# Kernel tuning notes

Hardware: AMD Instinct MI355X
Metric: run time of the kernel (lower is better)

The kernel has to match this reference:

```python
import jax, jax.numpy as jnp
import numpy as np

N = 100000       # nodes
E = 1600000      # edges (avg degree 16)
ND = 64          # node_dim
ED = 1           # edge_dim
HD = 128         # hidden_dim of message MLP


def setup_inputs() -> dict:
    key = jax.random.key(0)
    ks = jax.random.split(key, 12)
    x = jax.random.normal(ks[0], (N, ND), dtype=jnp.float32)
    edge_index = jax.random.randint(ks[1], (2, E), 0, N, dtype=jnp.int32)
    edge_attr = jax.random.normal(ks[2], (E, ED), dtype=jnp.float32)
    # message_net: Linear(2*ND+ED -> HD), ReLU, Linear(HD -> ND); torch default uniform init
    s1 = 1.0 / np.sqrt(2 * ND + ED)
    W1 = jax.random.uniform(ks[3], (HD, 2 * ND + ED), minval=-s1, maxval=s1, dtype=jnp.float32)
    b1 = jax.random.uniform(ks[4], (HD,), minval=-s1, maxval=s1, dtype=jnp.float32)
    s2 = 1.0 / np.sqrt(HD)
    W2 = jax.random.uniform(ks[5], (ND, HD), minval=-s2, maxval=s2, dtype=jnp.float32)
    b2 = jax.random.uniform(ks[6], (ND,), minval=-s2, maxval=s2, dtype=jnp.float32)
    # GRUCell(input=ND, hidden=ND): weight_ih [3*ND, ND], weight_hh [3*ND, ND]
    sg = 1.0 / np.sqrt(ND)
    W_ih = jax.random.uniform(ks[7], (3 * ND, ND), minval=-sg, maxval=sg, dtype=jnp.float32)
    b_ih = jax.random.uniform(ks[8], (3 * ND,), minval=-sg, maxval=sg, dtype=jnp.float32)
    W_hh = jax.random.uniform(ks[9], (3 * ND, ND), minval=-sg, maxval=sg, dtype=jnp.float32)
    b_hh = jax.random.uniform(ks[10], (3 * ND,), minval=-sg, maxval=sg, dtype=jnp.float32)
    return {"x": x, "edge_index": edge_index, "edge_attr": edge_attr,
            "W1": W1, "b1": b1, "W2": W2, "b2": b2,
            "W_ih": W_ih, "b_ih": b_ih, "W_hh": W_hh, "b_hh": b_hh}


def reference(x, edge_index, edge_attr, W1, b1, W2, b2, W_ih, b_ih, W_hh, b_hh):
    src, dst = edge_index[0], edge_index[1]
    # gather + concat + 2-layer MLP message  -> [E, ND]
    m = jnp.concatenate([x[src], x[dst], edge_attr], axis=-1)      # [E, 2*ND+ED]
    m = jax.nn.relu(m @ W1.T + b1) @ W2.T + b2                     # [E, ND]
    # scatter-add aggregate to destination nodes
    aggr = jnp.zeros_like(x).at[dst].add(m)                        # [N, ND]
    # torch GRUCell: input=aggr, hidden=x
    gi = aggr @ W_ih.T + b_ih                                      # [N, 3*ND]
    gh = x @ W_hh.T + b_hh                                         # [N, 3*ND]
    i_r, i_z, i_n = jnp.split(gi, 3, axis=-1)
    h_r, h_z, h_n = jnp.split(gh, 3, axis=-1)
    r = jax.nn.sigmoid(i_r + h_r)
    z = jax.nn.sigmoid(i_z + h_z)
    n = jnp.tanh(i_n + r * h_n)
    return (1.0 - z) * n + z * x
```

## Files before the change

kernel.cpp:

```cpp
#include <hip/hip_runtime.h>

#define NN 100000
#define NE 1600000
#define ND 64
#define HD 128
#define NPB 8
#define NBK (NN / NPB)
#define NPCB 400
#define NCB 250
#define NFPC (NPCB / NPB)
#define NBA 64
#define CHA (NE / NBA)
#define MSC (NCB * NBA)
#define CSC 16

typedef float f32x4 __attribute__((ext_vector_type(4)));
typedef short s16x8 __attribute__((ext_vector_type(8)));


static __device__ __forceinline__ short f2bf(float f) {
    union { float f; unsigned u; } v; v.f = f;
    unsigned r = (v.u + 0x7fffu + ((v.u >> 16) & 1u)) >> 16;
    return (short)r;
}

#define LSW(n, k)  (((n) << 7) + ((((k) >> 3) ^ ((n) & 15)) << 3) + ((k) & 7))
#define LSW64(n, k) (((n) << 6) + ((((k) >> 3) ^ ((n) & 7)) << 3) + ((k) & 7))

__global__ __launch_bounds__(1024) void histA(const int* __restrict__ ei,
                                              int* __restrict__ gHistA,
                                              const float* __restrict__ x,
                                              short* __restrict__ xb) {
    __shared__ int h[NCB];
    const int tid = threadIdx.x;
    if (tid < NCB) h[tid] = 0;
    __syncthreads();
    const int base = blockIdx.x * CHA;
    for (int i = tid; i < CHA; i += 1024)
        atomicAdd(&h[ei[NE + base + i] / NPCB], 1);
    __syncthreads();
    if (tid < NCB) gHistA[tid * NBA + blockIdx.x] = h[tid];

    const int NG = NN * ND / 8;
    for (int g = blockIdx.x * 1024 + tid; g < NG; g += NBA * 1024) {
        const float4 a = ((const float4*)x)[g * 2];
        const float4 b = ((const float4*)x)[g * 2 + 1];
        s16x8 o;
        o[0] = f2bf(a.x); o[1] = f2bf(a.y); o[2] = f2bf(a.z); o[3] = f2bf(a.w);
        o[4] = f2bf(b.x); o[5] = f2bf(b.y); o[6] = f2bf(b.z); o[7] = f2bf(b.w);
        ((s16x8*)xb)[g] = o;
    }
}

__global__ __launch_bounds__(1024) void scanA(int* __restrict__ g,
                                              int* __restrict__ ticket) {
    __shared__ int A[1024], B[1024];
    const int t  = threadIdx.x;
    const int i0 = t * CSC;
    const int i1 = min(i0 + CSC, MSC);
    int s = 0;
    for (int i = i0; i < i1; ++i) s += g[i];
    A[t] = s;
    __syncthreads();
    int* src = A; int* dst = B;
    for (int off = 1; off < 1024; off <<= 1) {
        int val = src[t];
        if (t >= off) val += src[t - off];
        dst[t] = val;
        __syncthreads();
        int* tmp = src; src = dst; dst = tmp;
    }
    int run = t ? src[t - 1] : 0;
    for (int i = i0; i < i1; ++i) {
        const int v = g[i];
        g[i] = run; run += v;
    }
    if (t == 0) *ticket = 0;
}

__global__ __launch_bounds__(1024) void scatterA(
    const int* __restrict__ ei, const float* __restrict__ ea,
    const int* __restrict__ gBaseA, int2* __restrict__ tsd) {
    __shared__ int cur[NCB];
    const int tid = threadIdx.x;
    if (tid < NCB) cur[tid] = gBaseA[tid * NBA + blockIdx.x];
    __syncthreads();
    const int base = blockIdx.x * CHA;
    for (int i = tid; i < CHA; i += 1024) {
        const int e = base + i;
        const int sv = ei[e], d = ei[NE + e];
        const float av = ea[e];
        const int c = d / NPCB;
        const int dloc = d - c * NPCB;
        const int pos = atomicAdd(&cur[c], 1);
        tsd[pos] = make_int2(sv | (dloc << 17), __float_as_int(av));
    }
}

__global__ __launch_bounds__(1024) void scatterB(
    const int2* __restrict__ tsd, const int* __restrict__ gBaseA,
    int2* __restrict__ rsd, int* __restrict__ rowptrB) {
    __shared__ int h[NPCB];
    __shared__ int cur[NPCB];
    __shared__ int A[512], B[512];
    const int c = blockIdx.x;
    const int t = threadIdx.x;
    const int nb0  = c * NPCB;
    const int base = gBaseA[c * NBA];
    const int endc = (c + 1 < NCB) ? gBaseA[(c + 1) * NBA] : NE;

    if (t < NPCB) h[t] = 0;
    __syncthreads();
    for (int i = base + t; i < endc; i += 1024)
        atomicAdd(&h[(tsd[i].x >> 17) & 0x1FF], 1);
    __syncthreads();

    if (t < 512) A[t] = (t < NPCB) ? h[t] : 0;
    __syncthreads();
    int* src = A; int* dst = B;
    for (int off = 1; off < 512; off <<= 1) {
        if (t < 512) {
            int val = src[t];
            if (t >= off) val += src[t - off];
            dst[t] = val;
        }
        __syncthreads();
        int* tmp = src; src = dst; dst = tmp;
    }
    if (t < NPCB) {
        const int excl = t ? src[t - 1] : 0;
        cur[t] = base + excl;
        if ((t & (NPB - 1)) == 0)
            rowptrB[(nb0 + t) / NPB] = base + excl;
    }
    if (c == NCB - 1 && t == 0) rowptrB[NBK] = NE;
    __syncthreads();

    for (int i = base + t; i < endc; i += 1024) {
        const int2 r = tsd[i];
        const int pos = atomicAdd(&cur[(r.x >> 17) & 0x1FF], 1);
        rsd[pos] = r;
    }
}

__global__ __launch_bounds__(512) void msg_mfma3(
    const short* __restrict__ xb, const int2* __restrict__ rsd,
    const int* __restrict__ rowptrB, int* __restrict__ ticket,
    const float* __restrict__ W1, const float* __restrict__ b1,
    const float* __restrict__ W2, const float* __restrict__ b2,
    float* __restrict__ aggr)
{
    __shared__ short w1lds[128 * 128];
    __shared__ short w2lds[64 * 128];
    __shared__ short vbuf[8 * 16 * 128];
    __shared__ float albuf[8 * NPB * 64];

    const int tid = threadIdx.x;
    for (int i = tid; i < 128 * 128; i += 512) {
        int n = i >> 7, k = i & 127;
        w1lds[LSW(n, k)] = f2bf(W1[n * 129 + k]);
    }
    for (int i = tid; i < 64 * 128; i += 512) {
        int n = i >> 7, k = i & 127;
        w2lds[LSW(n, k)] = f2bf(W2[n * 128 + k]);
    }
    __syncthreads();

    const int lane = tid & 63;
    const int w    = tid >> 6;
    const int nlo  = lane & 15;
    const int q    = lane >> 4;

    float w1l[8], b1v[8], b2v[4];
    #pragma unroll
    for (int t = 0; t < 8; ++t) {
        w1l[t] = W1[(nlo + 16 * t) * 129 + 128];
        b1v[t] = b1[nlo + 16 * t];
    }
    #pragma unroll
    for (int t = 0; t < 4; ++t) b2v[t] = b2[nlo + 16 * t];

    short* myv = vbuf + w * (16 * 128);
    float* vf  = (float*)myv;
    float* al  = albuf + w * (NPB * 64);

    for (;;) {
        int bk = 0;
        if (lane == 0) bk = atomicAdd(ticket, 1);
        bk = __shfl(bk, 0, 64);
        if (bk >= NBK) break;

        const int n0    = bk * NPB;
        const int cbase = (bk / NFPC) * NPCB;
        const int bdl   = (bk % NFPC) * NPB;
        const int start = rowptrB[bk];
        const int end   = rowptrB[bk + 1];

        const f32x4 z = {0.f, 0.f, 0.f, 0.f};
        #pragma unroll
        for (int j = 0; j < 2; ++j) ((f32x4*)al)[lane + 64 * j] = z;

        if (start < end) {
            int2 e0 = rsd[min(start + nlo, end - 1)];
            int2 e1 = rsd[min(start + 16 + nlo, end - 1)];
            const int sr0 = (e0.x & 0x1FFFF) * ND + (q << 3);
            const int dr0 = (cbase + ((e0.x >> 17) & 0x1FF)) * ND + (q << 3);
            s16x8 a0 = *(const s16x8*)(xb + sr0);
            s16x8 a1 = *(const s16x8*)(xb + sr0 + 32);
            s16x8 a2 = *(const s16x8*)(xb + dr0);
            s16x8 a3 = *(const s16x8*)(xb + dr0 + 32);

            for (int p = start; p < end; p += 16) {
                const int2 e2 = rsd[min(p + 32 + nlo, end - 1)];
                const int sr1 = (e1.x & 0x1FFFF) * ND + (q << 3);
                const int dr1 = (cbase + ((e1.x >> 17) & 0x1FF)) * ND + (q << 3);
                const s16x8 n0_ = *(const s16x8*)(xb + sr1);
                const s16x8 n1_ = *(const s16x8*)(xb + sr1 + 32);
                const s16x8 n2_ = *(const s16x8*)(xb + dr1);
                const s16x8 n3_ = *(const s16x8*)(xb + dr1 + 32);

                const int   dlv = (e0.x >> 17) & 0x1FF;
                const float eav = __int_as_float(e0.y);

                f32x4 acc[8];
                #pragma unroll
                for (int t = 0; t < 8; ++t) { acc[t][0] = b1v[t]; acc[t][1] = b1v[t]; acc[t][2] = b1v[t]; acc[t][3] = b1v[t]; }

                __builtin_amdgcn_s_setprio(1);
                #pragma unroll
                for (int kk = 0; kk < 4; ++kk) {
                    const s16x8 af = (kk == 0) ? a0 : (kk == 1) ? a1 : (kk == 2) ? a2 : a3;
                    const int chunk = ((kk * 4 + q) ^ nlo) << 3;
                    #pragma unroll
                    for (int t = 0; t < 8; ++t) {
                        const s16x8 bf = *(const s16x8*)(w1lds + ((nlo + 16 * t) << 7) + chunk);
                        acc[t] = __builtin_amdgcn_mfma_f32_16x16x32_bf16(af, bf, acc[t], 0, 0, 0);
                    }
                }
                __builtin_amdgcn_s_setprio(0);

                float ear[4];
                #pragma unroll
                for (int r = 0; r < 4; ++r) ear[r] = __shfl(eav, q * 4 + r, 64);
                #pragma unroll
                for (int t = 0; t < 8; ++t) {
                    #pragma unroll
                    for (int r = 0; r < 4; ++r) {
                        const float hv = fmaxf(acc[t][r] + ear[r] * w1l[t], 0.f);
                        const int m = q * 4 + r;
                        const int k = nlo + 16 * t;
                        myv[LSW(m, k)] = f2bf(hv);
                    }
                }

                f32x4 acc2[4];
                #pragma unroll
                for (int t = 0; t < 4; ++t) { acc2[t][0] = b2v[t]; acc2[t][1] = b2v[t]; acc2[t][2] = b2v[t]; acc2[t][3] = b2v[t]; }

                __builtin_amdgcn_s_setprio(1);
                #pragma unroll
                for (int kk = 0; kk < 4; ++kk) {
                    const int chunk = ((kk * 4 + q) ^ nlo) << 3;
                    const s16x8 af = *(const s16x8*)(myv + (nlo << 7) + chunk);
                    #pragma unroll
                    for (int t = 0; t < 4; ++t) {
                        const s16x8 bf = *(const s16x8*)(w2lds + ((nlo + 16 * t) << 7) + chunk);
                        acc2[t] = __builtin_amdgcn_mfma_f32_16x16x32_bf16(af, bf, acc2[t], 0, 0, 0);
                    }
                }
                __builtin_amdgcn_s_setprio(0);

                #pragma unroll
                for (int t = 0; t < 4; ++t) {
                    #pragma unroll
                    for (int r = 0; r < 4; ++r) {
                        const int m = q * 4 + r;
                        vf[m * 64 + ((nlo + 16 * t) ^ (q << 3))] = acc2[t][r];
                    }
                }

                const int nrows = min(16, end - p);
                float vals[16];
                #pragma unroll
                for (int r = 0; r < 16; ++r)
                    vals[r] = vf[r * 64 + (lane ^ ((r >> 2) << 3))];

                int   prev = __builtin_amdgcn_readlane(dlv, 0);
                float sum  = vals[0];
                #pragma unroll
                for (int r = 1; r < 16; ++r) {
                    if (r < nrows) {
                        const int dd = __builtin_amdgcn_readlane(dlv, r);
                        if (dd == prev) sum += vals[r];
                        else {
                            al[(prev - bdl) * 64 + lane] += sum;
                            prev = dd; sum = vals[r];
                        }
                    }
                }
                al[(prev - bdl) * 64 + lane] += sum;

                e0 = e1; e1 = e2;
                a0 = n0_; a1 = n1_; a2 = n2_; a3 = n3_;
            }
        }

        f32x4* dstv = (f32x4*)(aggr + n0 * 64);
        #pragma unroll
        for (int j = 0; j < 2; ++j)
            dstv[lane + 64 * j] = ((f32x4*)al)[lane + 64 * j];
    }
}

__global__ __launch_bounds__(512) void gru_mfma(
    const float* __restrict__ x, const float* __restrict__ aggr,
    const float* __restrict__ Wih, const float* __restrict__ bih,
    const float* __restrict__ Whh, const float* __restrict__ bhh,
    float* __restrict__ out)
{
    __shared__ short wi[192 * 64];
    __shared__ short wh[192 * 64];

    const int tid = threadIdx.x;
    for (int i = tid; i < 192 * 64; i += 512) {
        int n = i >> 6, k = i & 63;
        wi[LSW64(n, k)] = f2bf(Wih[n * 64 + k]);
        wh[LSW64(n, k)] = f2bf(Whh[n * 64 + k]);
    }
    __syncthreads();

    const int lane = tid & 63;
    const int w    = tid >> 6;
    const int nlo  = lane & 15;
    const int q    = lane >> 4;

    float bi[12], bh[12];
    #pragma unroll
    for (int t = 0; t < 12; ++t) { bi[t] = bih[16 * t + nlo]; bh[t] = bhh[16 * t + nlo]; }

    const int gw = blockIdx.x * 8 + w;
    const int nw = gridDim.x * 8;

    for (int tile = gw; tile < NN / 16; tile += nw) {
        const int n0 = tile * 16;
        f32x4 ai[12], ah[12];
        #pragma unroll
        for (int t = 0; t < 12; ++t) {
            ai[t][0] = bi[t]; ai[t][1] = bi[t]; ai[t][2] = bi[t]; ai[t][3] = bi[t];
            ah[t][0] = bh[t]; ah[t][1] = bh[t]; ah[t][2] = bh[t]; ah[t][3] = bh[t];
        }

        #pragma unroll
        for (int kk = 0; kk < 2; ++kk) {
            const int coff = (n0 + nlo) * ND + kk * 32 + q * 8;
            const float4 a0 = *(const float4*)(aggr + coff);
            const float4 a1 = *(const float4*)(aggr + coff + 4);
            const float4 x0 = *(const float4*)(x + coff);
            const float4 x1 = *(const float4*)(x + coff + 4);
            s16x8 fA, fX;
            fA[0] = f2bf(a0.x); fA[1] = f2bf(a0.y); fA[2] = f2bf(a0.z); fA[3] = f2bf(a0.w);
            fA[4] = f2bf(a1.x); fA[5] = f2bf(a1.y); fA[6] = f2bf(a1.z); fA[7] = f2bf(a1.w);
            fX[0] = f2bf(x0.x); fX[1] = f2bf(x0.y); fX[2] = f2bf(x0.z); fX[3] = f2bf(x0.w);
            fX[4] = f2bf(x1.x); fX[5] = f2bf(x1.y); fX[6] = f2bf(x1.z); fX[7] = f2bf(x1.w);
            const int chunk = kk * 4 + q;
            #pragma unroll
            for (int t = 0; t < 12; ++t) {
                const int rb = 16 * t + nlo;
                const int boff = (rb << 6) + (((chunk) ^ (rb & 7)) << 3);
                const s16x8 bI = *(const s16x8*)(wi + boff);
                const s16x8 bH = *(const s16x8*)(wh + boff);
                ai[t] = __builtin_amdgcn_mfma_f32_16x16x32_bf16(fA, bI, ai[t], 0, 0, 0);
                ah[t] = __builtin_amdgcn_mfma_f32_16x16x32_bf16(fX, bH, ah[t], 0, 0, 0);
            }
        }

        #pragma unroll
        for (int t = 0; t < 4; ++t) {
            #pragma unroll
            for (int r = 0; r < 4; ++r) {
                const int node = n0 + q * 4 + r;
                const int c    = nlo + 16 * t;
                const float rr = 1.f / (1.f + __expf(-(ai[t][r] + ah[t][r])));
                const float zz = 1.f / (1.f + __expf(-(ai[t + 4][r] + ah[t + 4][r])));
                const float nv = ai[t + 8][r] + rr * ah[t + 8][r];
                const float nn = 2.f / (1.f + __expf(-2.f * nv)) - 1.f;
                const float xv = x[node * ND + c];
                out[node * ND + c] = (1.f - zz) * nn + zz * xv;
            }
        }
    }
}

extern "C" void kernel_launch(void* const* d_in, const int* in_sizes, int n_in,
                              void* d_out, int out_size, void* d_ws, size_t ws_size,
                              hipStream_t stream) {
    const float* x   = (const float*)d_in[0];
    const int*   ei  = (const int*)d_in[1];
    const float* ea  = (const float*)d_in[2];
    const float* W1  = (const float*)d_in[3];
    const float* b1  = (const float*)d_in[4];
    const float* W2  = (const float*)d_in[5];
    const float* b2  = (const float*)d_in[6];
    const float* Wih = (const float*)d_in[7];
    const float* bih = (const float*)d_in[8];
    const float* Whh = (const float*)d_in[9];
    const float* bhh = (const float*)d_in[10];
    float* out = (float*)d_out;

    char* ws = (char*)d_ws;
    float* aggr    = (float*)(ws);
    int2*  tsd     = (int2*) (ws);
    short* xb      = (short*)(ws + 25600000);
    int2*  rsd     = (int2*) (ws + 38400000);
    int*   gHistA  = (int*)  (ws + 51200000);
    int*   rowptrB = (int*)  (ws + 51264000);
    int*   ticket  = (int*)  (ws + 51314004);

    hipLaunchKernelGGL(histA, dim3(NBA), dim3(1024), 0, stream, ei, gHistA, x, xb);
    hipLaunchKernelGGL(scanA, dim3(1), dim3(1024), 0, stream, gHistA, ticket);
    hipLaunchKernelGGL(scatterA, dim3(NBA), dim3(1024), 0, stream,
                       ei, ea, gHistA, tsd);
    hipLaunchKernelGGL(scatterB, dim3(NCB), dim3(1024), 0, stream,
                       tsd, gHistA, rsd, rowptrB);
    hipLaunchKernelGGL(msg_mfma3, dim3(256), dim3(512), 0, stream,
                       xb, rsd, rowptrB, ticket, W1, b1, W2, b2, aggr);
    hipLaunchKernelGGL(gru_mfma, dim3(512), dim3(512), 0, stream,
                       x, aggr, Wih, bih, Whh, bhh, out);
}
```

Before: 529.1 us.

## Halve hidden staging buffer, scatter via LDS atomics, double message-kernel grid

The message kernel now stages the ReLU hidden layer in two 64-wide halves. Each half feeds the second MFMA stage right away, which halves the per-wave staging buffer in LDS. The serial readlane-based segmented reduction over dst rows is replaced by direct LDS float atomicAdd into a swizzled per-bucket accumulator. The final copy-out is adjusted to that swizzle. The lower LDS footprint is meant to allow more resident blocks, so the grid goes from 256 to 512 blocks, at the cost of LDS atomic contention and extra MFMA dependency stalls between the halves.

```diff
diff --git a/kernel.cpp b/kernel.cpp
--- a/kernel.cpp
+++ b/kernel.cpp
@@ -152,7 +152,7 @@
 {
     __shared__ short w1lds[128 * 128];
     __shared__ short w2lds[64 * 128];
-    __shared__ short vbuf[8 * 16 * 128];
+    __shared__ short vbuf[8 * 16 * 64];
     __shared__ float albuf[8 * NPB * 64];
 
     const int tid = threadIdx.x;
@@ -180,8 +180,7 @@
     #pragma unroll
     for (int t = 0; t < 4; ++t) b2v[t] = b2[nlo + 16 * t];
 
-    short* myv = vbuf + w * (16 * 128);
-    float* vf  = (float*)myv;
+    short* myv = vbuf + w * (16 * 64);
     float* al  = albuf + w * (NPB * 64);
 
     for (;;) {
@@ -242,73 +241,65 @@
                 float ear[4];
                 #pragma unroll
                 for (int r = 0; r < 4; ++r) ear[r] = __shfl(eav, q * 4 + r, 64);
-                #pragma unroll
-                for (int t = 0; t < 8; ++t) {
+
+                f32x4 acc2[4];
+                #pragma unroll
+                for (int t = 0; t < 4; ++t) { acc2[t][0] = b2v[t]; acc2[t][1] = b2v[t]; acc2[t][2] = b2v[t]; acc2[t][3] = b2v[t]; }
+
+                #pragma unroll
+                for (int half = 0; half < 2; ++half) {
                     #pragma unroll
-                    for (int r = 0; r < 4; ++r) {
-                        const float hv = fmaxf(acc[t][r] + ear[r] * w1l[t], 0.f);
-                        const int m = q * 4 + r;
-                        const int k = nlo + 16 * t;
-                        myv[LSW(m, k)] = f2bf(hv);
+                    for (int tt = 0; tt < 4; ++tt) {
+                        const int t = half * 4 + tt;
+                        #pragma unroll
+                        for (int r = 0; r < 4; ++r) {
+                            const float hv = fmaxf(acc[t][r] + ear[r] * w1l[t], 0.f);
+                            const int m = q * 4 + r;
+                            myv[LSW64(m, nlo + 16 * tt)] = f2bf(hv);
+                        }
                     }
+                    __builtin_amdgcn_s_setprio(1);
+                    #pragma unroll
+                    for (int kkl = 0; kkl < 2; ++kkl) {
+                        const int achunk = ((kkl * 4 + q) ^ (nlo & 7)) << 3;
+                        const s16x8 af = *(const s16x8*)(myv + (nlo << 6) + achunk);
+                        const int kkg = half * 2 + kkl;
+                        const int bchunk = ((kkg * 4 + q) ^ nlo) << 3;
+                        #pragma unroll
+                        for (int t = 0; t < 4; ++t) {
+                            const s16x8 bf = *(const s16x8*)(w2lds + ((nlo + 16 * t) << 7) + bchunk);
+                            acc2[t] = __builtin_amdgcn_mfma_f32_16x16x32_bf16(af, bf, acc2[t], 0, 0, 0);
+                        }
+                    }
+                    __builtin_amdgcn_s_setprio(0);
                 }
 
-                f32x4 acc2[4];
-                #pragma unroll
-                for (int t = 0; t < 4; ++t) { acc2[t][0] = b2v[t]; acc2[t][1] = b2v[t]; acc2[t][2] = b2v[t]; acc2[t][3] = b2v[t]; }
-
-                __builtin_amdgcn_s_setprio(1);
-                #pragma unroll
-                for (int kk = 0; kk < 4; ++kk) {
-                    const int chunk = ((kk * 4 + q) ^ nlo) << 3;
-                    const s16x8 af = *(const s16x8*)(myv + (nlo << 7) + chunk);
-                    #pragma unroll
-                    for (int t = 0; t < 4; ++t) {
-                        const s16x8 bf = *(const s16x8*)(w2lds + ((nlo + 16 * t) << 7) + chunk);
-                        acc2[t] = __builtin_amdgcn_mfma_f32_16x16x32_bf16(af, bf, acc2[t], 0, 0, 0);
-                    }
-                }
-                __builtin_amdgcn_s_setprio(0);
-
+                int dl_[4];
+                #pragma unroll
+                for (int r = 0; r < 4; ++r) dl_[r] = __shfl(dlv, q * 4 + r, 64);
                 #pragma unroll
                 for (int t = 0; t < 4; ++t) {
                     #pragma unroll
                     for (int r = 0; r < 4; ++r) {
-                        const int m = q * 4 + r;
-                        vf[m * 64 + ((nlo + 16 * t) ^ (q << 3))] = acc2[t][r];
+                        const float v = (p + q * 4 + r < end) ? acc2[t][r] : 0.f;
+                        const int row = dl_[r] - bdl;
+                        atomicAdd(&al[row * 64 + (((t ^ (row & 3)) << 4) | nlo)], v);
                     }
                 }
-
-                const int nrows = min(16, end - p);
-                float vals[16];
-                #pragma unroll
-                for (int r = 0; r < 16; ++r)
-                    vals[r] = vf[r * 64 + (lane ^ ((r >> 2) << 3))];
-
-                int   prev = __builtin_amdgcn_readlane(dlv, 0);
-                float sum  = vals[0];
-                #pragma unroll
-                for (int r = 1; r < 16; ++r) {
-                    if (r < nrows) {
-                        const int dd = __builtin_amdgcn_readlane(dlv, r);
-                        if (dd == prev) sum += vals[r];
-                        else {
-                            al[(prev - bdl) * 64 + lane] += sum;
-                            prev = dd; sum = vals[r];
-                        }
-                    }
-                }
-                al[(prev - bdl) * 64 + lane] += sum;
 
                 e0 = e1; e1 = e2;
                 a0 = n0_; a1 = n1_; a2 = n2_; a3 = n3_;
             }
         }
 
-        f32x4* dstv = (f32x4*)(aggr + n0 * 64);
         #pragma unroll
-        for (int j = 0; j < 2; ++j)
-            dstv[lane + 64 * j] = ((f32x4*)al)[lane + 64 * j];
+        for (int j = 0; j < 2; ++j) {
+            const int i   = lane + 64 * j;
+            const int row = i >> 4;
+            const int c4  = (i & 15) * 4;
+            const f32x4 val = *(const f32x4*)(al + row * 64 + (c4 ^ ((row & 3) << 4)));
+            *(f32x4*)(aggr + (n0 + row) * 64 + c4) = val;
+        }
     }
 }
 
@@ -422,7 +413,7 @@
                        ei, ea, gHistA, tsd);
     hipLaunchKernelGGL(scatterB, dim3(NCB), dim3(1024), 0, stream,
                        tsd, gHistA, rsd, rowptrB);
-    hipLaunchKernelGGL(msg_mfma3, dim3(256), dim3(512), 0, stream,
+    hipLaunchKernelGGL(msg_mfma3, dim3(512), dim3(512), 0, stream,
                        xb, rsd, rowptrB, ticket, W1, b1, W2, b2, aggr);
     hipLaunchKernelGGL(gru_mfma, dim3(512), dim3(512), 0, stream,
                        x, aggr, Wih, bih, Whh, bhh, out);
```

Measured after the change: 995.4 us. +88.1%, slower.
